# Optimization experiments

Hardware: AMD Instinct MI355X
Metric: run time of the kernel (lower is better)

## Reference

```python
import jax, jax.numpy as jnp
import numpy as np

N_NODES = 50000
N_EDGES = 800000
IN_DIM, HID_DIM, OUT_DIM = 256, 256, 128


def gcn_conv(x, edge_index, W, b, num_nodes):
    """PyG GCNConv: self-loops + symmetric norm + linear + scatter-add + bias."""
    loop = jnp.arange(num_nodes, dtype=edge_index.dtype)
    src = jnp.concatenate([edge_index[0], loop])  # message sources
    dst = jnp.concatenate([edge_index[1], loop])  # message targets
    ones = jnp.ones(dst.shape[0], dtype=x.dtype)
    deg = jax.ops.segment_sum(ones, dst, num_segments=num_nodes)
    dinv = jnp.where(deg > 0, jax.lax.rsqrt(deg), 0.0)
    norm = dinv[src] * dinv[dst]                  # [E+N]
    h = x @ W                                     # [N, out]
    msg = h[src] * norm[:, None]                  # gather + scale, [E+N, out]
    out = jax.ops.segment_sum(msg, dst, num_segments=num_nodes)
    return out + b


def setup_inputs() -> dict:
    key = jax.random.key(0)
    k1, k2, k3, k4, k5, k6 = jax.random.split(key, 6)
    x = jax.random.normal(k1, (N_NODES, IN_DIM), dtype=jnp.float32)
    edge_index = jax.random.randint(k2, (2, N_EDGES), 0, N_NODES, dtype=jnp.int64)
    s1 = 1.0 / np.sqrt(IN_DIM)
    s2 = 1.0 / np.sqrt(HID_DIM)
    W1 = jax.random.uniform(k3, (IN_DIM, HID_DIM), jnp.float32, -s1, s1)
    b1 = jax.random.uniform(k4, (HID_DIM,), jnp.float32, -s1, s1)
    W2 = jax.random.uniform(k5, (HID_DIM, OUT_DIM), jnp.float32, -s2, s2)
    b2 = jax.random.uniform(k6, (OUT_DIM,), jnp.float32, -s2, s2)
    return {"x": x, "edge_index": edge_index, "W1": W1, "b1": b1, "W2": W2, "b2": b2}


def reference(x, edge_index, W1, b1, W2, b2):
    n = x.shape[0]
    h = jax.nn.relu(gcn_conv(x, edge_index, W1, b1, n))
    out = jax.nn.sigmoid(gcn_conv(h, edge_index, W2, b2, n))
    return out
```

## Files before the change

kernel.cpp:

```cpp
#include <hip/hip_runtime.h>
#include <hip/hip_bf16.h>
#include <math.h>

#define N_NODES 50000
#define N_EDGES 800000
#define D_IN 256
#define D_HID 256
#define D_OUT 128

typedef unsigned short ushort_t;
typedef unsigned char uchar_t;
typedef __attribute__((ext_vector_type(8))) short bf16x8;
typedef __attribute__((ext_vector_type(4))) float f32x4;

__device__ inline ushort_t f2bf(float f) {
    __hip_bfloat16 h = __float2bfloat16(f);
    return *reinterpret_cast<ushort_t*>(&h);
}
__device__ inline float blo(unsigned u) {
    union { unsigned i; float f; } v; v.i = u << 16; return v.f;
}
__device__ inline float bhi(unsigned u) {
    union { unsigned i; float f; } v; v.i = u & 0xffff0000u; return v.f;
}
__device__ inline uchar_t f2fp8(float a) {
    int w = __builtin_amdgcn_cvt_pk_fp8_f32(a, a, 0, false);
    return (uchar_t)(w & 0xff);
}
__device__ inline void fp8x4_to_f32(unsigned u, float* o) {
    auto p0 = __builtin_amdgcn_cvt_pk_f32_fp8(u, false);
    auto p1 = __builtin_amdgcn_cvt_pk_f32_fp8(u, true);
    o[0] = p0[0]; o[1] = p0[1]; o[2] = p1[0]; o[3] = p1[1];
}
__device__ inline void fp8x2_to_f32(unsigned u, float* o) {
    auto p0 = __builtin_amdgcn_cvt_pk_f32_fp8(u, false);
    o[0] = p0[0]; o[1] = p0[1];
}

#define NODES_PER_GRP 6250


__global__ __launch_bounds__(256) void k_count_convW(const int* __restrict__ dst,
                                                     int* __restrict__ degI,
                                                     const float* __restrict__ W1,
                                                     const float* __restrict__ W2,
                                                     ushort_t* __restrict__ Wt1,
                                                     ushort_t* __restrict__ Wt2,
                                                     uchar_t* __restrict__ h1z,
                                                     uchar_t* __restrict__ h2z) {
    const int b = blockIdx.x;
    if (b < 512) {
        const int g = b & 7;
        const int slice = b >> 3;
        const int lo = g * NODES_PER_GRP, hi = lo + NODES_PER_GRP;
        const int i0 = slice * 12500;
        for (int i = i0 + threadIdx.x; i < i0 + 12500; i += 256) {
            const int d = dst[i];
            if (d >= lo && d < hi) atomicAdd(&degI[d], 1);
        }
    } else {
        int i = (b - 512) * 256 + threadIdx.x;
        const int n1 = D_IN * D_HID;
        const int n2 = D_HID * D_OUT;
        if (i < n1) {
            int k = i / D_HID, n = i % D_HID;
            Wt1[(size_t)n * D_IN + k] = f2bf(W1[i]);
        } else if (i < n1 + n2) {
            int j = i - n1;
            int k = j / D_OUT, n = j % D_OUT;
            Wt2[(size_t)n * D_HID + k] = f2bf(W2[j]);
        } else {
            int j = i - n1 - n2;
            if (j < D_HID) h1z[j] = 0;
            else if (j < D_HID + D_OUT) h2z[j - D_HID] = 0;
        }
    }
}


__global__ __launch_bounds__(256) void k_scan_apply(const int* __restrict__ degI,
                                                    int* __restrict__ offs,
                                                    int* __restrict__ cursor,
                                                    float* __restrict__ dinv,
                                                    ushort_t* __restrict__ ebuf, int n) {
    __shared__ int s[256];
    const int t = threadIdx.x;
    const int b = blockIdx.x;

    int pre = 0;
    const int lim = b * 256;
    for (int i = t; i < lim; i += 256) pre += (degI[i] + 15) & ~15;
    s[t] = pre;
    __syncthreads();
    for (int st = 128; st > 0; st >>= 1) {
        if (t < st) s[t] += s[t + st];
        __syncthreads();
    }
    const int blockoff = s[0];
    __syncthreads();

    const int i = b * 256 + t;
    const int deg = (i < n) ? degI[i] : 0;
    const int v = (deg + 15) & ~15;
    s[t] = v;
    __syncthreads();
    for (int off = 1; off < 256; off <<= 1) {
        int u = 0;
        if (t >= off) u = s[t - off];
        __syncthreads();
        if (t >= off) s[t] += u;
        __syncthreads();
    }
    const int excl = s[t] - v + blockoff;
    if (i < n) {
        offs[i] = excl;
        cursor[i] = excl;
        dinv[i] = rsqrtf((float)(1 + deg));
        for (int p = excl + deg; p < excl + v; ++p) ebuf[p] = (ushort_t)N_NODES;
        if (i == n - 1) offs[n] = excl + v;
    }
}


__global__ __launch_bounds__(512) void k_fill_gemm1(const int* __restrict__ src,
                                                    const int* __restrict__ dst,
                                                    int* __restrict__ cursor,
                                                    ushort_t* __restrict__ ebuf,
                                                    const float* __restrict__ A,
                                                    const ushort_t* __restrict__ Bt,
                                                    const float* __restrict__ dinvD,
                                                    uchar_t* __restrict__ C,
                                                    int M, int gemmBlocks) {
    __shared__ ushort_t As[128 * 40];
    __shared__ ushort_t Bs[256 * 40];

    if (blockIdx.x >= gemmBlocks) {
        const int fb = blockIdx.x - gemmBlocks;
        const int g = fb & 7;
        const int slice = fb >> 3;
        const int lo = g * NODES_PER_GRP, hi = lo + NODES_PER_GRP;
        const int i0 = slice * 4000;
        for (int i = i0 + threadIdx.x; i < i0 + 4000; i += 512) {
            const int d = dst[i];
            if (d >= lo && d < hi) {
                const int pos = atomicAdd(&cursor[d], 1);
                ebuf[pos] = (ushort_t)src[i];
            }
        }
        return;
    }

    const int t = threadIdx.x;
    const int lane = t & 63;
    const int w = t >> 6;
    const int wr = w >> 2;
    const int wc = w & 3;
    const int m0 = blockIdx.x * 128;

    const int arow = t >> 2;
    const int acol = (t & 3) * 8;
    const int brow = t >> 1;
    const int bcol = (t & 1) * 16;

    f32x4 acc[4][4];
#pragma unroll
    for (int m = 0; m < 4; ++m)
#pragma unroll
        for (int n = 0; n < 4; ++n)
#pragma unroll
            for (int i = 0; i < 4; ++i) acc[m][n][i] = 0.0f;

    for (int kt = 0; kt < 256; kt += 32) {
        {
            const int gr = m0 + arow;
            float4 v0 = make_float4(0.f, 0.f, 0.f, 0.f);
            float4 v1 = make_float4(0.f, 0.f, 0.f, 0.f);
            if (gr < M) {
                const float* p = A + (size_t)gr * 256 + kt + acol;
                v0 = *(const float4*)p;
                v1 = *(const float4*)(p + 4);
            }
            ushort4 u0, u1;
            u0.x = f2bf(v0.x); u0.y = f2bf(v0.y); u0.z = f2bf(v0.z); u0.w = f2bf(v0.w);
            u1.x = f2bf(v1.x); u1.y = f2bf(v1.y); u1.z = f2bf(v1.z); u1.w = f2bf(v1.w);
            *(ushort4*)&As[arow * 40 + acol] = u0;
            *(ushort4*)&As[arow * 40 + acol + 4] = u1;
        }
        {
            const uint4* p = (const uint4*)(Bt + (size_t)brow * 256 + kt + bcol);
            uint4 v0 = p[0], v1 = p[1];
            *(uint4*)&Bs[brow * 40 + bcol] = v0;
            *(uint4*)&Bs[brow * 40 + bcol + 8] = v1;
        }
        __syncthreads();

        const int kg = (lane >> 4) * 8;
        const int lr = lane & 15;
        bf16x8 a[4], b[4];
#pragma unroll
        for (int m = 0; m < 4; ++m)
            a[m] = *(const bf16x8*)&As[(wr * 64 + m * 16 + lr) * 40 + kg];
#pragma unroll
        for (int n = 0; n < 4; ++n)
            b[n] = *(const bf16x8*)&Bs[(wc * 64 + n * 16 + lr) * 40 + kg];
#pragma unroll
        for (int m = 0; m < 4; ++m)
#pragma unroll
            for (int n = 0; n < 4; ++n)
                acc[m][n] = __builtin_amdgcn_mfma_f32_16x16x32_bf16(a[m], b[n], acc[m][n], 0, 0, 0);
        __syncthreads();
    }

    const int lr = lane & 15;
    const int rg = (lane >> 4) * 4;
#pragma unroll
    for (int m = 0; m < 4; ++m) {
        const int rb = m0 + wr * 64 + m * 16 + rg;
#pragma unroll
        for (int i = 0; i < 4; ++i) {
            const int row = rb + i;
            if (row < M) {
                const float dr = dinvD[row];
#pragma unroll
                for (int n = 0; n < 4; ++n) {
                    const int col = wc * 64 + n * 16 + lr;
                    C[(size_t)row * 256 + col] = f2fp8(acc[m][n][i] * dr);
                }
            }
        }
    }
}


__global__ __launch_bounds__(256) void k_gemm2(const ushort_t* __restrict__ A,
                                               const ushort_t* __restrict__ Bt,
                                               const float* __restrict__ dinvD,
                                               uchar_t* __restrict__ C, int M) {
    __shared__ ushort_t As[128 * 40];
    __shared__ ushort_t Bs[128 * 40];

    const int t = threadIdx.x;
    const int lane = t & 63;
    const int w = t >> 6;
    const int wr = w >> 1, wc = w & 1;
    const int m0 = blockIdx.x * 128;

    const int srow = t >> 1;
    const int scol = (t & 1) * 16;

    f32x4 acc[4][4];
#pragma unroll
    for (int m = 0; m < 4; ++m)
#pragma unroll
        for (int n = 0; n < 4; ++n)
#pragma unroll
            for (int i = 0; i < 4; ++i) acc[m][n][i] = 0.0f;

    for (int kt = 0; kt < 256; kt += 32) {
        {
            const int gr = m0 + srow;
            uint4 v0 = make_uint4(0, 0, 0, 0), v1 = make_uint4(0, 0, 0, 0);
            if (gr < M) {
                const uint4* p = (const uint4*)(A + (size_t)gr * 256 + kt + scol);
                v0 = p[0]; v1 = p[1];
            }
            *(uint4*)&As[srow * 40 + scol] = v0;
            *(uint4*)&As[srow * 40 + scol + 8] = v1;
        }
        {
            const uint4* p = (const uint4*)(Bt + (size_t)srow * 256 + kt + scol);
            uint4 v0 = p[0], v1 = p[1];
            *(uint4*)&Bs[srow * 40 + scol] = v0;
            *(uint4*)&Bs[srow * 40 + scol + 8] = v1;
        }
        __syncthreads();

        const int kg = (lane >> 4) * 8;
        const int lr = lane & 15;
        bf16x8 a[4], b[4];
#pragma unroll
        for (int m = 0; m < 4; ++m)
            a[m] = *(const bf16x8*)&As[(wr * 64 + m * 16 + lr) * 40 + kg];
#pragma unroll
        for (int n = 0; n < 4; ++n)
            b[n] = *(const bf16x8*)&Bs[(wc * 64 + n * 16 + lr) * 40 + kg];
#pragma unroll
        for (int m = 0; m < 4; ++m)
#pragma unroll
            for (int n = 0; n < 4; ++n)
                acc[m][n] = __builtin_amdgcn_mfma_f32_16x16x32_bf16(a[m], b[n], acc[m][n], 0, 0, 0);
        __syncthreads();
    }

    const int lr = lane & 15;
    const int rg = (lane >> 4) * 4;
#pragma unroll
    for (int m = 0; m < 4; ++m) {
        const int rb = m0 + wr * 64 + m * 16 + rg;
#pragma unroll
        for (int i = 0; i < 4; ++i) {
            const int row = rb + i;
            if (row < M) {
                const float dr = dinvD[row];
#pragma unroll
                for (int n = 0; n < 4; ++n) {
                    const int col = wc * 64 + n * 16 + lr;
                    C[(size_t)row * 128 + col] = f2fp8(acc[m][n][i] * dr);
                }
            }
        }
    }
}


__device__ inline void ld_idx16u(const ushort_t* __restrict__ p, int* s) {
    uint4 a = ((const uint4*)p)[0];
    uint4 b = ((const uint4*)p)[1];
    unsigned w0 = __builtin_amdgcn_readfirstlane(a.x);
    unsigned w1 = __builtin_amdgcn_readfirstlane(a.y);
    unsigned w2 = __builtin_amdgcn_readfirstlane(a.z);
    unsigned w3 = __builtin_amdgcn_readfirstlane(a.w);
    unsigned w4 = __builtin_amdgcn_readfirstlane(b.x);
    unsigned w5 = __builtin_amdgcn_readfirstlane(b.y);
    unsigned w6 = __builtin_amdgcn_readfirstlane(b.z);
    unsigned w7 = __builtin_amdgcn_readfirstlane(b.w);
    s[0]  = w0 & 0xffff; s[1]  = w0 >> 16;
    s[2]  = w1 & 0xffff; s[3]  = w1 >> 16;
    s[4]  = w2 & 0xffff; s[5]  = w2 >> 16;
    s[6]  = w3 & 0xffff; s[7]  = w3 >> 16;
    s[8]  = w4 & 0xffff; s[9]  = w4 >> 16;
    s[10] = w5 & 0xffff; s[11] = w5 >> 16;
    s[12] = w6 & 0xffff; s[13] = w6 >> 16;
    s[14] = w7 & 0xffff; s[15] = w7 >> 16;
}


__global__ __launch_bounds__(256) void k_gather_fp8(const uchar_t* __restrict__ h,
                                                    const float* __restrict__ dinv,
                                                    const int* __restrict__ offs,
                                                    const ushort_t* __restrict__ ebuf,
                                                    const float* __restrict__ bias,
                                                    ushort_t* __restrict__ out, int n) {
    const int node = (blockIdx.x * 256 + threadIdx.x) >> 6;
    const int lane = threadIdx.x & 63;
    if (node >= n) return;

    const int base = lane * 4;
    const uchar_t* hb = h + base;
    const float di = dinv[node];

    float acc[4];
    {
        const unsigned u = *(const unsigned*)(hb + (size_t)node * D_HID);
        fp8x4_to_f32(u, acc);
    }

    int e = __builtin_amdgcn_readfirstlane(offs[node]);
    const int e1 = __builtin_amdgcn_readfirstlane(offs[node + 1]);

    int cs[16], ns[16];
    bool have = e < e1;
    if (have) ld_idx16u(ebuf + e, cs);

    while (have) {
        const int en = e + 16;
        const bool hn = en < e1;
        unsigned u[16];
#pragma unroll
        for (int j = 0; j < 16; ++j)
            u[j] = *(const unsigned*)(hb + (size_t)cs[j] * D_HID);
        if (hn) ld_idx16u(ebuf + en, ns);
#pragma unroll
        for (int j = 0; j < 16; ++j) {
            float d[4];
            fp8x4_to_f32(u[j], d);
            acc[0] += d[0]; acc[1] += d[1]; acc[2] += d[2]; acc[3] += d[3];
        }
        e = en; have = hn;
#pragma unroll
        for (int j = 0; j < 16; ++j) cs[j] = ns[j];
    }

    ushort4 o;
    o.x = f2bf(fmaxf(di * acc[0] + bias[base + 0], 0.f));
    o.y = f2bf(fmaxf(di * acc[1] + bias[base + 1], 0.f));
    o.z = f2bf(fmaxf(di * acc[2] + bias[base + 2], 0.f));
    o.w = f2bf(fmaxf(di * acc[3] + bias[base + 3], 0.f));
    *(ushort4*)(out + (size_t)node * D_HID + base) = o;
}


__global__ __launch_bounds__(256) void k_gather_fp8_2(const uchar_t* __restrict__ h,
                                                      const float* __restrict__ dinv,
                                                      const int* __restrict__ offs,
                                                      const ushort_t* __restrict__ ebuf,
                                                      const float* __restrict__ bias,
                                                      float* __restrict__ out, int n) {
    const int node = (blockIdx.x * 256 + threadIdx.x) >> 6;
    const int lane = threadIdx.x & 63;
    if (node >= n) return;

    const int base = lane * 2;
    const uchar_t* hb = h + base;
    const float di = dinv[node];

    float acc[2];
    {
        const unsigned u = *(const ushort_t*)(hb + (size_t)node * D_OUT);
        fp8x2_to_f32(u, acc);
    }

    int e = __builtin_amdgcn_readfirstlane(offs[node]);
    const int e1 = __builtin_amdgcn_readfirstlane(offs[node + 1]);

    int cs[16], ns[16];
    bool have = e < e1;
    if (have) ld_idx16u(ebuf + e, cs);

    while (have) {
        const int en = e + 16;
        const bool hn = en < e1;
        unsigned u[16];
#pragma unroll
        for (int j = 0; j < 16; ++j)
            u[j] = *(const ushort_t*)(hb + (size_t)cs[j] * D_OUT);
        if (hn) ld_idx16u(ebuf + en, ns);
#pragma unroll
        for (int j = 0; j < 16; ++j) {
            float d[2];
            fp8x2_to_f32(u[j], d);
            acc[0] += d[0]; acc[1] += d[1];
        }
        e = en; have = hn;
#pragma unroll
        for (int j = 0; j < 16; ++j) cs[j] = ns[j];
    }

    const float v0 = di * acc[0] + bias[base + 0];
    const float v1 = di * acc[1] + bias[base + 1];
    float2 r;
    r.x = 1.0f / (1.0f + expf(-v0));
    r.y = 1.0f / (1.0f + expf(-v1));
    *(float2*)(out + (size_t)node * D_OUT + base) = r;
}


extern "C" void kernel_launch(void* const* d_in, const int* in_sizes, int n_in,
                              void* d_out, int out_size, void* d_ws, size_t ws_size,
                              hipStream_t stream) {
    const float* x  = (const float*)d_in[0];
    const int*   ei = (const int*)d_in[1];
    const float* W1 = (const float*)d_in[2];
    const float* b1 = (const float*)d_in[3];
    const float* W2 = (const float*)d_in[4];
    const float* b2 = (const float*)d_in[5];
    float* out = (float*)d_out;

    float* wsf    = (float*)d_ws;
    float* dinv   = wsf;
    int*   degI   = (int*)(wsf + 50048);
    int*   offs   = degI + 50048;
    int*   cursor = offs + 50064;
    ushort_t* ebuf= (ushort_t*)(cursor + 50048);
    ushort_t* Wt1 = ebuf + 1600000;
    ushort_t* Wt2 = Wt1 + 65536;
    uchar_t*  h1  = (uchar_t*)(Wt2 + 32768);
    ushort_t* agg1= (ushort_t*)(h1 + (size_t)50048 * D_HID);
    uchar_t*  h2  = (uchar_t*)(agg1 + (size_t)50048 * D_HID);

    const int* src = ei;
    const int* dst = ei + N_EDGES;

    const int blocksN = (N_NODES + 255) / 256;

    hipMemsetAsync(degI, 0, N_NODES * sizeof(int), stream);

    k_count_convW<<<512 + 386, 256, 0, stream>>>(dst, degI, W1, W2, Wt1, Wt2,
                                                 h1 + (size_t)N_NODES * D_HID,
                                                 h2 + (size_t)N_NODES * D_OUT);

    k_scan_apply<<<blocksN, 256, 0, stream>>>(degI, offs, cursor, dinv, ebuf, N_NODES);

    {
        const int gemmBlocks = (N_NODES + 127) / 128;
        k_fill_gemm1<<<gemmBlocks + 1600, 512, 0, stream>>>(
            src, dst, cursor, ebuf, x, Wt1, dinv, h1, N_NODES, gemmBlocks);
    }

    k_gather_fp8<<<(N_NODES * 64 + 255) / 256, 256, 0, stream>>>(
        h1, dinv, offs, ebuf, b1, agg1, N_NODES);

    k_gemm2<<<(N_NODES + 127) / 128, 256, 0, stream>>>(agg1, Wt2, dinv, h2, N_NODES);

    k_gather_fp8_2<<<(N_NODES * 64 + 255) / 256, 256, 0, stream>>>(
        h2, dinv, offs, ebuf, b2, out, N_NODES);
}
```

Baseline: 205.0 us.

## Fuse layer-1 aggregation into layer-2 GEMM via shared-memory tile

Merges the first-layer gather/aggregation kernel with the second GEMM. Each block aggregates 64 nodes into a bf16 tile held in LDS, then multiplies that tile by W2 with MFMA and writes fp8 h2. This removes the agg1 round trip through global memory and one kernel launch. In exchange, the gather runs with fewer waves in flight, since each wave handles 16 nodes serially. The larger LDS footprint may also lower occupancy and hurt latency hiding for the random gathers.

```diff
diff --git a/kernel.cpp b/kernel.cpp
--- a/kernel.cpp
+++ b/kernel.cpp
@@ -16,12 +16,6 @@
 __device__ inline ushort_t f2bf(float f) {
     __hip_bfloat16 h = __float2bfloat16(f);
     return *reinterpret_cast<ushort_t*>(&h);
-}
-__device__ inline float blo(unsigned u) {
-    union { unsigned i; float f; } v; v.i = u << 16; return v.f;
-}
-__device__ inline float bhi(unsigned u) {
-    union { unsigned i; float f; } v; v.i = u & 0xffff0000u; return v.f;
 }
 __device__ inline uchar_t f2fp8(float a) {
     int w = __builtin_amdgcn_cvt_pk_fp8_f32(a, a, 0, false);
@@ -225,87 +219,6 @@
                 for (int n = 0; n < 4; ++n) {
                     const int col = wc * 64 + n * 16 + lr;
                     C[(size_t)row * 256 + col] = f2fp8(acc[m][n][i] * dr);
-                }
-            }
-        }
-    }
-}
-
-
-__global__ __launch_bounds__(256) void k_gemm2(const ushort_t* __restrict__ A,
-                                               const ushort_t* __restrict__ Bt,
-                                               const float* __restrict__ dinvD,
-                                               uchar_t* __restrict__ C, int M) {
-    __shared__ ushort_t As[128 * 40];
-    __shared__ ushort_t Bs[128 * 40];
-
-    const int t = threadIdx.x;
-    const int lane = t & 63;
-    const int w = t >> 6;
-    const int wr = w >> 1, wc = w & 1;
-    const int m0 = blockIdx.x * 128;
-
-    const int srow = t >> 1;
-    const int scol = (t & 1) * 16;
-
-    f32x4 acc[4][4];
-#pragma unroll
-    for (int m = 0; m < 4; ++m)
-#pragma unroll
-        for (int n = 0; n < 4; ++n)
-#pragma unroll
-            for (int i = 0; i < 4; ++i) acc[m][n][i] = 0.0f;
-
-    for (int kt = 0; kt < 256; kt += 32) {
-        {
-            const int gr = m0 + srow;
-            uint4 v0 = make_uint4(0, 0, 0, 0), v1 = make_uint4(0, 0, 0, 0);
-            if (gr < M) {
-                const uint4* p = (const uint4*)(A + (size_t)gr * 256 + kt + scol);
-                v0 = p[0]; v1 = p[1];
-            }
-            *(uint4*)&As[srow * 40 + scol] = v0;
-            *(uint4*)&As[srow * 40 + scol + 8] = v1;
-        }
-        {
-            const uint4* p = (const uint4*)(Bt + (size_t)srow * 256 + kt + scol);
-            uint4 v0 = p[0], v1 = p[1];
-            *(uint4*)&Bs[srow * 40 + scol] = v0;
-            *(uint4*)&Bs[srow * 40 + scol + 8] = v1;
-        }
-        __syncthreads();
-
-        const int kg = (lane >> 4) * 8;
-        const int lr = lane & 15;
-        bf16x8 a[4], b[4];
-#pragma unroll
-        for (int m = 0; m < 4; ++m)
-            a[m] = *(const bf16x8*)&As[(wr * 64 + m * 16 + lr) * 40 + kg];
-#pragma unroll
-        for (int n = 0; n < 4; ++n)
-            b[n] = *(const bf16x8*)&Bs[(wc * 64 + n * 16 + lr) * 40 + kg];
-#pragma unroll
-        for (int m = 0; m < 4; ++m)
-#pragma unroll
-            for (int n = 0; n < 4; ++n)
-                acc[m][n] = __builtin_amdgcn_mfma_f32_16x16x32_bf16(a[m], b[n], acc[m][n], 0, 0, 0);
-        __syncthreads();
-    }
-
-    const int lr = lane & 15;
-    const int rg = (lane >> 4) * 4;
-#pragma unroll
-    for (int m = 0; m < 4; ++m) {
-        const int rb = m0 + wr * 64 + m * 16 + rg;
-#pragma unroll
-        for (int i = 0; i < 4; ++i) {
-            const int row = rb + i;
-            if (row < M) {
-                const float dr = dinvD[row];
-#pragma unroll
-                for (int n = 0; n < 4; ++n) {
-                    const int col = wc * 64 + n * 16 + lr;
-                    C[(size_t)row * 128 + col] = f2fp8(acc[m][n][i] * dr);
                 }
             }
         }
@@ -335,58 +248,121 @@
 }
 
 
-__global__ __launch_bounds__(256) void k_gather_fp8(const uchar_t* __restrict__ h,
-                                                    const float* __restrict__ dinv,
-                                                    const int* __restrict__ offs,
-                                                    const ushort_t* __restrict__ ebuf,
-                                                    const float* __restrict__ bias,
-                                                    ushort_t* __restrict__ out, int n) {
-    const int node = (blockIdx.x * 256 + threadIdx.x) >> 6;
-    const int lane = threadIdx.x & 63;
-    if (node >= n) return;
+__global__ __launch_bounds__(256) void k_agg_gemm2(const uchar_t* __restrict__ h,
+                                                   const float* __restrict__ dinv,
+                                                   const int* __restrict__ offs,
+                                                   const ushort_t* __restrict__ ebuf,
+                                                   const float* __restrict__ bias,
+                                                   const ushort_t* __restrict__ Bt,
+                                                   uchar_t* __restrict__ h2, int n) {
+    __shared__ ushort_t As[64 * 264];
+    __shared__ ushort_t Bs[128 * 40];
+
+    const int t = threadIdx.x;
+    const int lane = t & 63;
+    const int w = t >> 6;
+    const int m0 = blockIdx.x * 64;
 
     const int base = lane * 4;
     const uchar_t* hb = h + base;
-    const float di = dinv[node];
-
-    float acc[4];
-    {
-        const unsigned u = *(const unsigned*)(hb + (size_t)node * D_HID);
-        fp8x4_to_f32(u, acc);
-    }
-
-    int e = __builtin_amdgcn_readfirstlane(offs[node]);
-    const int e1 = __builtin_amdgcn_readfirstlane(offs[node + 1]);
-
-    int cs[16], ns[16];
-    bool have = e < e1;
-    if (have) ld_idx16u(ebuf + e, cs);
-
-    while (have) {
-        const int en = e + 16;
-        const bool hn = en < e1;
-        unsigned u[16];
-#pragma unroll
-        for (int j = 0; j < 16; ++j)
-            u[j] = *(const unsigned*)(hb + (size_t)cs[j] * D_HID);
-        if (hn) ld_idx16u(ebuf + en, ns);
-#pragma unroll
-        for (int j = 0; j < 16; ++j) {
-            float d[4];
-            fp8x4_to_f32(u[j], d);
-            acc[0] += d[0]; acc[1] += d[1]; acc[2] += d[2]; acc[3] += d[3];
-        }
-        e = en; have = hn;
-#pragma unroll
-        for (int j = 0; j < 16; ++j) cs[j] = ns[j];
-    }
-
-    ushort4 o;
-    o.x = f2bf(fmaxf(di * acc[0] + bias[base + 0], 0.f));
-    o.y = f2bf(fmaxf(di * acc[1] + bias[base + 1], 0.f));
-    o.z = f2bf(fmaxf(di * acc[2] + bias[base + 2], 0.f));
-    o.w = f2bf(fmaxf(di * acc[3] + bias[base + 3], 0.f));
-    *(ushort4*)(out + (size_t)node * D_HID + base) = o;
+
+    for (int i = 0; i < 16; ++i) {
+        const int row = w * 16 + i;
+        const int node = m0 + row;
+        if (node < n) {
+            float acc[4];
+            {
+                const unsigned u = *(const unsigned*)(hb + (size_t)node * D_HID);
+                fp8x4_to_f32(u, acc);
+            }
+            int e = __builtin_amdgcn_readfirstlane(offs[node]);
+            const int e1 = __builtin_amdgcn_readfirstlane(offs[node + 1]);
+            int cs[16], ns[16];
+            bool have = e < e1;
+            if (have) ld_idx16u(ebuf + e, cs);
+            while (have) {
+                const int en = e + 16;
+                const bool hn = en < e1;
+                unsigned u[16];
+#pragma unroll
+                for (int j = 0; j < 16; ++j)
+                    u[j] = *(const unsigned*)(hb + (size_t)cs[j] * D_HID);
+                if (hn) ld_idx16u(ebuf + en, ns);
+#pragma unroll
+                for (int j = 0; j < 16; ++j) {
+                    float d[4];
+                    fp8x4_to_f32(u[j], d);
+                    acc[0] += d[0]; acc[1] += d[1]; acc[2] += d[2]; acc[3] += d[3];
+                }
+                e = en; have = hn;
+#pragma unroll
+                for (int j = 0; j < 16; ++j) cs[j] = ns[j];
+            }
+            const float di = dinv[node];
+            ushort4 o;
+            o.x = f2bf(fmaxf(di * acc[0] + bias[base + 0], 0.f));
+            o.y = f2bf(fmaxf(di * acc[1] + bias[base + 1], 0.f));
+            o.z = f2bf(fmaxf(di * acc[2] + bias[base + 2], 0.f));
+            o.w = f2bf(fmaxf(di * acc[3] + bias[base + 3], 0.f));
+            *(ushort4*)&As[row * 264 + base] = o;
+        }
+    }
+    __syncthreads();
+
+    const int lr = lane & 15;
+    const int kg = (lane >> 4) * 8;
+    const int wc = w;
+
+    f32x4 acc2[4][2];
+#pragma unroll
+    for (int m = 0; m < 4; ++m)
+#pragma unroll
+        for (int nn = 0; nn < 2; ++nn)
+#pragma unroll
+            for (int i = 0; i < 4; ++i) acc2[m][nn][i] = 0.0f;
+
+    for (int kt = 0; kt < 256; kt += 32) {
+        {
+            const int srow = t >> 1;
+            const int scol = (t & 1) * 16;
+            const uint4* p = (const uint4*)(Bt + (size_t)srow * 256 + kt + scol);
+            uint4 v0 = p[0], v1 = p[1];
+            *(uint4*)&Bs[srow * 40 + scol] = v0;
+            *(uint4*)&Bs[srow * 40 + scol + 8] = v1;
+        }
+        __syncthreads();
+
+        bf16x8 a[4], b[2];
+#pragma unroll
+        for (int m = 0; m < 4; ++m)
+            a[m] = *(const bf16x8*)&As[(m * 16 + lr) * 264 + kt + kg];
+#pragma unroll
+        for (int nn = 0; nn < 2; ++nn)
+            b[nn] = *(const bf16x8*)&Bs[(wc * 32 + nn * 16 + lr) * 40 + kg];
+#pragma unroll
+        for (int m = 0; m < 4; ++m)
+#pragma unroll
+            for (int nn = 0; nn < 2; ++nn)
+                acc2[m][nn] = __builtin_amdgcn_mfma_f32_16x16x32_bf16(a[m], b[nn], acc2[m][nn], 0, 0, 0);
+        __syncthreads();
+    }
+
+    const int rg = (lane >> 4) * 4;
+#pragma unroll
+    for (int m = 0; m < 4; ++m) {
+#pragma unroll
+        for (int i = 0; i < 4; ++i) {
+            const int gr = m0 + m * 16 + rg + i;
+            if (gr < n) {
+                const float dr = dinv[gr];
+#pragma unroll
+                for (int nn = 0; nn < 2; ++nn) {
+                    const int col = wc * 32 + nn * 16 + lr;
+                    h2[(size_t)gr * 128 + col] = f2fp8(acc2[m][nn][i] * dr);
+                }
+            }
+        }
+    }
 }
 
 
@@ -465,8 +441,7 @@
     ushort_t* Wt1 = ebuf + 1600000;
     ushort_t* Wt2 = Wt1 + 65536;
     uchar_t*  h1  = (uchar_t*)(Wt2 + 32768);
-    ushort_t* agg1= (ushort_t*)(h1 + (size_t)50048 * D_HID);
-    uchar_t*  h2  = (uchar_t*)(agg1 + (size_t)50048 * D_HID);
+    uchar_t*  h2  = h1 + (size_t)50048 * D_HID;
 
     const int* src = ei;
     const int* dst = ei + N_EDGES;
@@ -487,10 +462,8 @@
             src, dst, cursor, ebuf, x, Wt1, dinv, h1, N_NODES, gemmBlocks);
     }
 
-    k_gather_fp8<<<(N_NODES * 64 + 255) / 256, 256, 0, stream>>>(
-        h1, dinv, offs, ebuf, b1, agg1, N_NODES);
-
-    k_gemm2<<<(N_NODES + 127) / 128, 256, 0, stream>>>(agg1, Wt2, dinv, h2, N_NODES);
+    k_agg_gemm2<<<(N_NODES + 63) / 64, 256, 0, stream>>>(
+        h1, dinv, offs, ebuf, b1, Wt2, h2, N_NODES);
 
     k_gather_fp8_2<<<(N_NODES * 64 + 255) / 256, 256, 0, stream>>>(
         h2, dinv, offs, ebuf, b2, out, N_NODES);
```

Result: slower. 223.6 us (+9.1%).
